# Performance work log

Hardware: AMD Instinct MI355X
Metric: run time of the kernel (lower is better)

## Reference

```python
import jax, jax.numpy as jnp
import numpy as np

HEADS = 8
DIM_HEAD = 64
SMOOTH = 1e-4
BN_EPS = 1e-5


def setup_inputs() -> dict:
    key = jax.random.key(0)
    k1, k2, k3 = jax.random.split(key, 3)
    B, C, H, W = 1, 256, 64, 64
    inner = HEADS * DIM_HEAD  # 512
    x = jax.random.normal(k1, (B, C, H, W), dtype=jnp.float32)
    # 1x1 conv weights stored as [out_ch, in_ch]
    w_qkv = jax.random.normal(k2, (3 * inner, C), dtype=jnp.float32) * (1.0 / np.sqrt(C))
    w_out = jax.random.normal(k3, (C, inner), dtype=jnp.float32) * (1.0 / np.sqrt(inner))
    gamma = jnp.ones((C,), dtype=jnp.float32)
    beta = jnp.zeros((C,), dtype=jnp.float32)
    return {"x": x, "w_qkv": w_qkv, "w_out": w_out, "gamma": gamma, "beta": beta}


def reference(x, w_qkv, w_out, gamma, beta):
    B, C, H, W = x.shape
    n = H * W
    # 1x1 conv == channel matmul: [B,3*inner,H,W]
    qkv = jnp.einsum('bchw,oc->bohw', x, w_qkv)
    q, k, v = jnp.split(qkv, 3, axis=1)

    def to_heads(t):
        # b (g d) h w -> b g (h w) d
        return t.reshape(B, HEADS, DIM_HEAD, n).transpose(0, 1, 3, 2)

    q, k, v = to_heads(q), to_heads(k), to_heads(v)
    # cosine-style normalized attention (no softmax)
    attn = jnp.einsum('bgnd,bgmd->bgnm', q, k)  # [B,g,n,n]
    qn = jnp.sqrt(jnp.sum(q * q, axis=-1) + SMOOTH)  # [B,g,n]
    kn = jnp.sqrt(jnp.sum(k * k, axis=-1) + SMOOTH)  # [B,g,n]
    attn = attn / (qn[:, :, :, None] * kn[:, :, None, :] + SMOOTH)
    out = jnp.einsum('bgnm,bgmd->bgnd', attn, v)  # [B,g,n,d]
    # b g (h w) d -> b (g d) h w
    out = out.transpose(0, 1, 3, 2).reshape(B, HEADS * DIM_HEAD, H, W)
    # projection conv 1x1 + BatchNorm2d (training stats) + ReLU
    out = jnp.einsum('bchw,oc->bohw', out, w_out)
    mean = jnp.mean(out, axis=(0, 2, 3), keepdims=True)
    var = jnp.var(out, axis=(0, 2, 3), keepdims=True)
    out = (out - mean) / jnp.sqrt(var + BN_EPS)
    out = out * gamma[None, :, None, None] + beta[None, :, None, None]
    return jax.nn.relu(out)
```

## Files before the change

### kernel.cpp

```cpp
#include <hip/hip_runtime.h>
#include <hip/hip_bf16.h>

#define NSP   4096
#define CIN   256
#define INNER 512
#define QKV_ROWS 1536

typedef __attribute__((ext_vector_type(8))) short bf16x8;
typedef __attribute__((ext_vector_type(4))) float f32x4;

__global__ __launch_bounds__(256) void conv_weights(
    const float* __restrict__ w_qkv, const float* __restrict__ w_out,
    __hip_bfloat16* __restrict__ dq, __hip_bfloat16* __restrict__ do_)
{
    const int gid = blockIdx.x * 256 + threadIdx.x;
    const int i = gid * 8;
    const float* src;
    __hip_bfloat16* dst;
    int off;
    if (i < QKV_ROWS * CIN) { src = w_qkv; dst = dq;  off = i; }
    else                    { src = w_out; dst = do_; off = i - QKV_ROWS * CIN; }
    const float4 a = *(const float4*)(src + off);
    const float4 b = *(const float4*)(src + off + 4);
    alignas(16) __hip_bfloat16 t[8];
    t[0] = __float2bfloat16(a.x); t[1] = __float2bfloat16(a.y);
    t[2] = __float2bfloat16(a.z); t[3] = __float2bfloat16(a.w);
    t[4] = __float2bfloat16(b.x); t[5] = __float2bfloat16(b.y);
    t[6] = __float2bfloat16(b.z); t[7] = __float2bfloat16(b.w);
    *(uint4*)(dst + off) = *(const uint4*)t;
}

__global__ __launch_bounds__(256) void transpose_convert(
    const float* __restrict__ x, __hip_bfloat16* __restrict__ xT)
{
    __shared__ float t[64][65];
    const int n0 = blockIdx.x * 64, c0 = blockIdx.y * 64;
    const int tid = threadIdx.x;
    const int cl = tid >> 2, nl0 = (tid & 3) * 16;
    #pragma unroll
    for (int j = 0; j < 4; ++j) {
        const float4 v = *(const float4*)(x + (size_t)(c0 + cl) * NSP + n0 + nl0 + j * 4);
        t[cl][nl0 + j*4 + 0] = v.x; t[cl][nl0 + j*4 + 1] = v.y;
        t[cl][nl0 + j*4 + 2] = v.z; t[cl][nl0 + j*4 + 3] = v.w;
    }
    __syncthreads();
    const int nr = tid >> 2, cc0 = (tid & 3) * 16;
    alignas(16) __hip_bfloat16 tmp[16];
    #pragma unroll
    for (int j = 0; j < 16; ++j) tmp[j] = __float2bfloat16(t[cc0 + j][nr]);
    __hip_bfloat16* d = xT + (size_t)(n0 + nr) * CIN + c0 + cc0;
    *(uint4*)(d)     = ((const uint4*)tmp)[0];
    *(uint4*)(d + 8) = ((const uint4*)tmp)[1];
}

template<int K, int BM, int FR, int DO_NORMS>
__global__ __launch_bounds__(256) void gemm_bf16(
    const __hip_bfloat16* __restrict__ A,
    const __hip_bfloat16* __restrict__ BT,
    __hip_bfloat16* __restrict__ C, int Nstride,
    float* __restrict__ inv_qn, float* __restrict__ inv_kn,
    __hip_bfloat16* __restrict__ qT)
{
    __shared__ __hip_bfloat16 smem[(BM + 128) * 64];
    __hip_bfloat16* As = smem;
    __hip_bfloat16* Bs = smem + BM * 64;
    const int tid = threadIdx.x;
    const int w = tid >> 6, l = tid & 63;
    const int wr = w >> 1, wc = w & 1;
    const int row0 = blockIdx.y * BM, col0 = blockIdx.x * 128;

    f32x4 acc[FR][4];
    #pragma unroll
    for (int i = 0; i < FR; ++i)
        #pragma unroll
        for (int j = 0; j < 4; ++j)
            acc[i][j] = (f32x4){0.f, 0.f, 0.f, 0.f};

    for (int kt = 0; kt < K; kt += 64) {
        #pragma unroll
        for (int i = 0; i < BM / 32; ++i) {
            const int o = i * 4096 + w * 1024 + l * 16;
            const int r_ = o >> 7;
            const int kel = ((o & 127) ^ ((r_ & 7) << 4)) >> 1;
            __builtin_amdgcn_global_load_lds(
                (const __attribute__((address_space(1))) void*)(A + (size_t)(row0 + r_) * K + kt + kel),
                (__attribute__((address_space(3))) void*)((char*)As + o),
                16, 0, 0);
        }
        #pragma unroll
        for (int i = 0; i < 4; ++i) {
            const int o = i * 4096 + w * 1024 + l * 16;
            const int r_ = o >> 7;
            const int kel = ((o & 127) ^ ((r_ & 7) << 4)) >> 1;
            __builtin_amdgcn_global_load_lds(
                (const __attribute__((address_space(1))) void*)(BT + (size_t)(col0 + r_) * K + kt + kel),
                (__attribute__((address_space(3))) void*)((char*)Bs + o),
                16, 0, 0);
        }
        __syncthreads();

        #pragma unroll
        for (int ks = 0; ks < 2; ++ks) {
            bf16x8 af[FR], bfr[4];
            #pragma unroll
            for (int fr = 0; fr < FR; ++fr) {
                const int row = wr * FR * 16 + fr * 16 + (l & 15);
                const int addr = row * 128 + ((ks * 64 + ((l >> 4) * 16)) ^ ((row & 7) << 4));
                af[fr] = *(const bf16x8*)((const char*)As + addr);
            }
            #pragma unroll
            for (int fc = 0; fc < 4; ++fc) {
                const int col = wc * 64 + fc * 16 + (l & 15);
                const int addr = col * 128 + ((ks * 64 + ((l >> 4) * 16)) ^ ((col & 7) << 4));
                bfr[fc] = *(const bf16x8*)((const char*)Bs + addr);
            }
            #pragma unroll
            for (int fr = 0; fr < FR; ++fr)
                #pragma unroll
                for (int fc = 0; fc < 4; ++fc)
                    acc[fr][fc] = __builtin_amdgcn_mfma_f32_16x16x32_bf16(
                        af[fr], bfr[fc], acc[fr][fc], 0, 0, 0);
        }
        __syncthreads();
    }

    #pragma unroll
    for (int fr = 0; fr < FR; ++fr)
        #pragma unroll
        for (int fc = 0; fc < 4; ++fc)
            #pragma unroll
            for (int r = 0; r < 4; ++r) {
                const int row = row0 + wr * FR * 16 + fr * 16 + (l >> 4) * 4 + r;
                const int col = col0 + wc * 64 + fc * 16 + (l & 15);
                C[(size_t)row * Nstride + col] = __float2bfloat16(acc[fr][fc][r]);
            }

    if constexpr (DO_NORMS) {
        const int chbase = row0 + wr * 64;
        if (chbase < 1024) {
            const int head = chbase >> 6;
            #pragma unroll
            for (int fc = 0; fc < 4; ++fc) {
                float s = 0.f;
                #pragma unroll
                for (int fr = 0; fr < FR; ++fr)
                    #pragma unroll
                    for (int r = 0; r < 4; ++r)
                        s += acc[fr][fc][r] * acc[fr][fc][r];
                s += __shfl_xor(s, 16, 64);
                s += __shfl_xor(s, 32, 64);
                if ((l >> 4) == 0) {
                    const int col = col0 + wc * 64 + fc * 16 + l;
                    const float inv = rsqrtf(s + 1e-4f);
                    if (head < 8) inv_qn[head * NSP + col] = inv;
                    else          inv_kn[(head - 8) * NSP + col] = inv;
                }
            }
        }
        if (chbase < 512) {
            #pragma unroll
            for (int fr = 0; fr < FR; ++fr)
                #pragma unroll
                for (int fc = 0; fc < 4; ++fc) {
                    const int rowb = chbase + fr * 16 + (l >> 4) * 4;
                    const int col  = col0 + wc * 64 + fc * 16 + (l & 15);
                    alignas(8) __hip_bfloat16 t4[4];
                    #pragma unroll
                    for (int r = 0; r < 4; ++r) t4[r] = __float2bfloat16(acc[fr][fc][r]);
                    *(unsigned long long*)(qT + (size_t)col * INNER + rowb) =
                        *(const unsigned long long*)t4;
                }
        }
    }
}

__device__ inline bf16x8 scale8(bf16x8 a, float4 s0, float4 s1) {
    union { bf16x8 v; unsigned short u[8]; } in, out;
    in.v = a;
    const float s[8] = {s0.x, s0.y, s0.z, s0.w, s1.x, s1.y, s1.z, s1.w};
    #pragma unroll
    for (int j = 0; j < 8; ++j) {
        const float f = __uint_as_float(((unsigned)(unsigned short)in.u[j]) << 16) * s[j];
        const __hip_bfloat16 h = __float2bfloat16(f);
        out.u[j] = *(const unsigned short*)&h;
    }
    return out.v;
}

__global__ __launch_bounds__(256) void s_mfma(
    const __hip_bfloat16* __restrict__ qkv, const float* __restrict__ inv_kn,
    float* __restrict__ S_part)
{
    const int c = blockIdx.x, g = blockIdx.y;
    const int tid = threadIdx.x;
    const int w = tid >> 6, l = tid & 63;
    const __hip_bfloat16* kb = qkv + (size_t)(512 + g * 64 + w * 16 + (l & 15)) * NSP;
    const float* ikn = inv_kn + g * NSP;

    f32x4 acc[4];
    #pragma unroll
    for (int j = 0; j < 4; ++j) acc[j] = (f32x4){0.f, 0.f, 0.f, 0.f};

    #pragma unroll
    for (int s8 = 0; s8 < 4; ++s8) {
        const int na = c * 128 + s8 * 32 + (l >> 4) * 8;
        bf16x8 a = *(const bf16x8*)(kb + na);
        const float4 i0 = *(const float4*)(ikn + na);
        const float4 i1 = *(const float4*)(ikn + na + 4);
        a = scale8(a, i0, i1);
        #pragma unroll
        for (int fc = 0; fc < 4; ++fc) {
            const bf16x8 b = *(const bf16x8*)(
                qkv + (size_t)(1024 + g * 64 + fc * 16 + (l & 15)) * NSP + na);
            acc[fc] = __builtin_amdgcn_mfma_f32_16x16x32_bf16(a, b, acc[fc], 0, 0, 0);
        }
    }
    float* out = S_part + (size_t)(c * 8 + g) * 4096;
    #pragma unroll
    for (int fc = 0; fc < 4; ++fc)
        #pragma unroll
        for (int r = 0; r < 4; ++r)
            out[(w * 16 + (l >> 4) * 4 + r) * 64 + fc * 16 + (l & 15)] = acc[fc][r];
}

__global__ __launch_bounds__(256) void s_reduce(
    const float* __restrict__ S_part, __hip_bfloat16* __restrict__ SbT)
{
    const int t = blockIdx.x * 256 + threadIdx.x;
    const int g = t >> 12, rem = t & 4095;
    const int d1 = rem >> 6, d2 = rem & 63;
    float s = 0.f;
    #pragma unroll
    for (int c = 0; c < 32; ++c)
        s += S_part[(size_t)(c * 8 + g) * 4096 + d1 * 64 + d2];
    SbT[g * 4096 + d2 * 64 + d1] = __float2bfloat16(s);
}

__global__ __launch_bounds__(256) void av_mfma(
    const __hip_bfloat16* __restrict__ qT, const float* __restrict__ inv_qn,
    const __hip_bfloat16* __restrict__ SbT, __hip_bfloat16* __restrict__ attnT)
{
    const int nb = blockIdx.x, g = blockIdx.y;
    const int tid = threadIdx.x;
    const int w = tid >> 6, l = tid & 63;
    const int nwave = nb * 256 + w * 64;

    bf16x8 bfr[2][4];
    #pragma unroll
    for (int ks = 0; ks < 2; ++ks)
        #pragma unroll
        for (int fc = 0; fc < 4; ++fc)
            bfr[ks][fc] = *(const bf16x8*)(
                SbT + g * 4096 + (fc * 16 + (l & 15)) * 64 + ks * 32 + (l >> 4) * 8);

    #pragma unroll
    for (int mr = 0; mr < 4; ++mr) {
        f32x4 acc[4];
        #pragma unroll
        for (int j = 0; j < 4; ++j) acc[j] = (f32x4){0.f, 0.f, 0.f, 0.f};
        #pragma unroll
        for (int ks = 0; ks < 2; ++ks) {
            const bf16x8 a = *(const bf16x8*)(
                qT + (size_t)(nwave + mr * 16 + (l & 15)) * INNER + g * 64 + ks * 32 + (l >> 4) * 8);
            #pragma unroll
            for (int fc = 0; fc < 4; ++fc)
                acc[fc] = __builtin_amdgcn_mfma_f32_16x16x32_bf16(a, bfr[ks][fc], acc[fc], 0, 0, 0);
        }
        const int nrow = nwave + mr * 16 + (l >> 4) * 4;
        const float4 iq = *(const float4*)(inv_qn + g * NSP + nrow);
        const float iqa[4] = {iq.x, iq.y, iq.z, iq.w};
        #pragma unroll
        for (int fc = 0; fc < 4; ++fc)
            #pragma unroll
            for (int r = 0; r < 4; ++r)
                attnT[(size_t)(nrow + r) * INNER + g * 64 + fc * 16 + (l & 15)] =
                    __float2bfloat16(acc[fc][r] * iqa[r]);
    }
}

__global__ __launch_bounds__(256) void bn_fused(
    const __hip_bfloat16* __restrict__ proj,
    const float* __restrict__ gamma, const float* __restrict__ beta,
    float* __restrict__ out)
{
    const int c = blockIdx.x;
    const int tid = threadIdx.x;
    const __hip_bfloat16* p = proj + (size_t)c * NSP + tid * 16;
    float v[16];
    {
        const uint4 u0 = *(const uint4*)(p);
        const uint4 u1 = *(const uint4*)(p + 8);
        const __hip_bfloat16* b0 = (const __hip_bfloat16*)&u0;
        const __hip_bfloat16* b1 = (const __hip_bfloat16*)&u1;
        #pragma unroll
        for (int j = 0; j < 8; ++j) { v[j] = __bfloat162float(b0[j]); v[8 + j] = __bfloat162float(b1[j]); }
    }
    float s = 0.f, q = 0.f;
    #pragma unroll
    for (int j = 0; j < 16; ++j) { s += v[j]; q += v[j] * v[j]; }
    #pragma unroll
    for (int m = 1; m < 64; m <<= 1) { s += __shfl_xor(s, m, 64); q += __shfl_xor(q, m, 64); }
    __shared__ float ss[4], qq[4];
    if ((tid & 63) == 0) { ss[tid >> 6] = s; qq[tid >> 6] = q; }
    __syncthreads();
    s = ss[0] + ss[1] + ss[2] + ss[3];
    q = qq[0] + qq[1] + qq[2] + qq[3];
    const float mean = s * (1.f / 4096.f);
    const float var  = q * (1.f / 4096.f) - mean * mean;
    const float scal = rsqrtf(var + 1e-5f) * gamma[c];
    const float bb   = beta[c];
    float* o = out + (size_t)c * NSP + tid * 16;
    #pragma unroll
    for (int j = 0; j < 16; j += 4) {
        float4 r;
        r.x = (v[j+0] - mean) * scal + bb; r.x = r.x > 0.f ? r.x : 0.f;
        r.y = (v[j+1] - mean) * scal + bb; r.y = r.y > 0.f ? r.y : 0.f;
        r.z = (v[j+2] - mean) * scal + bb; r.z = r.z > 0.f ? r.z : 0.f;
        r.w = (v[j+3] - mean) * scal + bb; r.w = r.w > 0.f ? r.w : 0.f;
        *(float4*)(o + j) = r;
    }
}

extern "C" void kernel_launch(void* const* d_in, const int* in_sizes, int n_in,
                              void* d_out, int out_size, void* d_ws, size_t ws_size,
                              hipStream_t stream)
{
    const float* x      = (const float*)d_in[0];
    const float* w_qkv  = (const float*)d_in[1];
    const float* w_out  = (const float*)d_in[2];
    const float* gamma  = (const float*)d_in[3];
    const float* beta   = (const float*)d_in[4];
    float* out = (float*)d_out;

    char* ws = (char*)d_ws;
    __hip_bfloat16* qkv_bf  = (__hip_bfloat16*)ws;
    __hip_bfloat16* xT_bf   = (__hip_bfloat16*)(ws + 12582912);
    __hip_bfloat16* wqkv_bf = (__hip_bfloat16*)(ws + 14680064);
    __hip_bfloat16* wout_bf = (__hip_bfloat16*)(ws + 15466496);
    __hip_bfloat16* attnT   = (__hip_bfloat16*)(ws + 15728640);
    __hip_bfloat16* proj_bf = (__hip_bfloat16*)(ws + 19922944);
    float* inv_qn           = (float*)(ws + 22020096);
    float* inv_kn           = (float*)(ws + 22151168);
    __hip_bfloat16* qT      = (__hip_bfloat16*)(ws + 22282240);
    float* S_part           = (float*)(ws + 26476544);
    __hip_bfloat16* SbT     = (__hip_bfloat16*)(ws + 30670848);

    conv_weights<<<(QKV_ROWS * CIN + CIN * INNER) / 2048, 256, 0, stream>>>(
        w_qkv, w_out, wqkv_bf, wout_bf);
    transpose_convert<<<dim3(NSP / 64, CIN / 64), 256, 0, stream>>>(x, xT_bf);

    gemm_bf16<CIN, 128, 4, 1><<<dim3(NSP / 128, QKV_ROWS / 128), 256, 0, stream>>>(
        wqkv_bf, xT_bf, qkv_bf, NSP, inv_qn, inv_kn, qT);

    s_mfma<<<dim3(32, 8), 256, 0, stream>>>(qkv_bf, inv_kn, S_part);

    s_reduce<<<128, 256, 0, stream>>>(S_part, SbT);

    av_mfma<<<dim3(16, 8), 256, 0, stream>>>(qT, inv_qn, SbT, attnT);

    gemm_bf16<INNER, 64, 2, 0><<<dim3(NSP / 128, CIN / 64), 256, 0, stream>>>(
        wout_bf, attnT, proj_bf, NSP, nullptr, nullptr, nullptr);

    bn_fused<<<CIN, 256, 0, stream>>>(proj_bf, gamma, beta, out);
}
```

Baseline: 105.5 us.

## Fold q/k norm scaling into QKV GEMM epilogue and merge prep kernels

Merges the weight-conversion and input-transpose kernels into a single prep launch. The q/k inverse norms are now applied directly in the QKV GEMM epilogue rather than written to separate buffers and reapplied in s_mfma and av_mfma. This removes the inv_qn/inv_kn buffers, their reads and the per-element rescale in s_mfma. s_mfma is also changed to use half as many blocks, each doing twice the work, so s_reduce sums 16 partials instead of 32. The trade-off is lower parallelism in s_mfma. Q/K are rounded to bf16 after scaling rather than before, and the dropped ‑1e-4 term in the denominator is ignored.

Result: no change. 104.3 us (-1.2%).

```diff
diff --git a/kernel.cpp b/kernel.cpp
--- a/kernel.cpp
+++ b/kernel.cpp
@@ -9,48 +9,48 @@
 typedef __attribute__((ext_vector_type(8))) short bf16x8;
 typedef __attribute__((ext_vector_type(4))) float f32x4;
 
-__global__ __launch_bounds__(256) void conv_weights(
-    const float* __restrict__ w_qkv, const float* __restrict__ w_out,
-    __hip_bfloat16* __restrict__ dq, __hip_bfloat16* __restrict__ do_)
-{
-    const int gid = blockIdx.x * 256 + threadIdx.x;
-    const int i = gid * 8;
-    const float* src;
-    __hip_bfloat16* dst;
-    int off;
-    if (i < QKV_ROWS * CIN) { src = w_qkv; dst = dq;  off = i; }
-    else                    { src = w_out; dst = do_; off = i - QKV_ROWS * CIN; }
-    const float4 a = *(const float4*)(src + off);
-    const float4 b = *(const float4*)(src + off + 4);
-    alignas(16) __hip_bfloat16 t[8];
-    t[0] = __float2bfloat16(a.x); t[1] = __float2bfloat16(a.y);
-    t[2] = __float2bfloat16(a.z); t[3] = __float2bfloat16(a.w);
-    t[4] = __float2bfloat16(b.x); t[5] = __float2bfloat16(b.y);
-    t[6] = __float2bfloat16(b.z); t[7] = __float2bfloat16(b.w);
-    *(uint4*)(dst + off) = *(const uint4*)t;
-}
-
-__global__ __launch_bounds__(256) void transpose_convert(
-    const float* __restrict__ x, __hip_bfloat16* __restrict__ xT)
+__global__ __launch_bounds__(256) void prep(
+    const float* __restrict__ x, const float* __restrict__ w_qkv,
+    const float* __restrict__ w_out,
+    __hip_bfloat16* __restrict__ xT, __hip_bfloat16* __restrict__ wq,
+    __hip_bfloat16* __restrict__ wo)
 {
     __shared__ float t[64][65];
-    const int n0 = blockIdx.x * 64, c0 = blockIdx.y * 64;
-    const int tid = threadIdx.x;
-    const int cl = tid >> 2, nl0 = (tid & 3) * 16;
-    #pragma unroll
-    for (int j = 0; j < 4; ++j) {
-        const float4 v = *(const float4*)(x + (size_t)(c0 + cl) * NSP + n0 + nl0 + j * 4);
-        t[cl][nl0 + j*4 + 0] = v.x; t[cl][nl0 + j*4 + 1] = v.y;
-        t[cl][nl0 + j*4 + 2] = v.z; t[cl][nl0 + j*4 + 3] = v.w;
-    }
-    __syncthreads();
-    const int nr = tid >> 2, cc0 = (tid & 3) * 16;
-    alignas(16) __hip_bfloat16 tmp[16];
-    #pragma unroll
-    for (int j = 0; j < 16; ++j) tmp[j] = __float2bfloat16(t[cc0 + j][nr]);
-    __hip_bfloat16* d = xT + (size_t)(n0 + nr) * CIN + c0 + cc0;
-    *(uint4*)(d)     = ((const uint4*)tmp)[0];
-    *(uint4*)(d + 8) = ((const uint4*)tmp)[1];
+    const int bx = blockIdx.x;
+    const int tid = threadIdx.x;
+    if (bx < 256) {
+        const int n0 = (bx & 63) * 64, c0 = (bx >> 6) * 64;
+        const int cl = tid >> 2, nl0 = (tid & 3) * 16;
+        #pragma unroll
+        for (int j = 0; j < 4; ++j) {
+            const float4 v = *(const float4*)(x + (size_t)(c0 + cl) * NSP + n0 + nl0 + j * 4);
+            t[cl][nl0 + j*4 + 0] = v.x; t[cl][nl0 + j*4 + 1] = v.y;
+            t[cl][nl0 + j*4 + 2] = v.z; t[cl][nl0 + j*4 + 3] = v.w;
+        }
+        __syncthreads();
+        const int nr = tid >> 2, cc0 = (tid & 3) * 16;
+        alignas(16) __hip_bfloat16 tmp[16];
+        #pragma unroll
+        for (int j = 0; j < 16; ++j) tmp[j] = __float2bfloat16(t[cc0 + j][nr]);
+        __hip_bfloat16* d = xT + (size_t)(n0 + nr) * CIN + c0 + cc0;
+        *(uint4*)(d)     = ((const uint4*)tmp)[0];
+        *(uint4*)(d + 8) = ((const uint4*)tmp)[1];
+    } else {
+        const int i = ((bx - 256) * 256 + tid) * 8;
+        const float* src;
+        __hip_bfloat16* dst;
+        int off;
+        if (i < QKV_ROWS * CIN) { src = w_qkv; dst = wq; off = i; }
+        else                    { src = w_out; dst = wo; off = i - QKV_ROWS * CIN; }
+        const float4 a = *(const float4*)(src + off);
+        const float4 b = *(const float4*)(src + off + 4);
+        alignas(16) __hip_bfloat16 tt[8];
+        tt[0] = __float2bfloat16(a.x); tt[1] = __float2bfloat16(a.y);
+        tt[2] = __float2bfloat16(a.z); tt[3] = __float2bfloat16(a.w);
+        tt[4] = __float2bfloat16(b.x); tt[5] = __float2bfloat16(b.y);
+        tt[6] = __float2bfloat16(b.z); tt[7] = __float2bfloat16(b.w);
+        *(uint4*)(dst + off) = *(const uint4*)tt;
+    }
 }
 
 template<int K, int BM, int FR, int DO_NORMS>
@@ -58,7 +58,6 @@
     const __hip_bfloat16* __restrict__ A,
     const __hip_bfloat16* __restrict__ BT,
     __hip_bfloat16* __restrict__ C, int Nstride,
-    float* __restrict__ inv_qn, float* __restrict__ inv_kn,
     __hip_bfloat16* __restrict__ qT)
 {
     __shared__ __hip_bfloat16 smem[(BM + 128) * 64];
@@ -124,21 +123,10 @@
         __syncthreads();
     }
 
-    #pragma unroll
-    for (int fr = 0; fr < FR; ++fr)
-        #pragma unroll
-        for (int fc = 0; fc < 4; ++fc)
-            #pragma unroll
-            for (int r = 0; r < 4; ++r) {
-                const int row = row0 + wr * FR * 16 + fr * 16 + (l >> 4) * 4 + r;
-                const int col = col0 + wc * 64 + fc * 16 + (l & 15);
-                C[(size_t)row * Nstride + col] = __float2bfloat16(acc[fr][fc][r]);
-            }
-
     if constexpr (DO_NORMS) {
         const int chbase = row0 + wr * 64;
+        float inv[4] = {1.f, 1.f, 1.f, 1.f};
         if (chbase < 1024) {
-            const int head = chbase >> 6;
             #pragma unroll
             for (int fc = 0; fc < 4; ++fc) {
                 float s = 0.f;
@@ -149,12 +137,7 @@
                         s += acc[fr][fc][r] * acc[fr][fc][r];
                 s += __shfl_xor(s, 16, 64);
                 s += __shfl_xor(s, 32, 64);
-                if ((l >> 4) == 0) {
-                    const int col = col0 + wc * 64 + fc * 16 + l;
-                    const float inv = rsqrtf(s + 1e-4f);
-                    if (head < 8) inv_qn[head * NSP + col] = inv;
-                    else          inv_kn[(head - 8) * NSP + col] = inv;
-                }
+                inv[fc] = rsqrtf(s + 1e-4f);
             }
         }
         if (chbase < 512) {
@@ -166,52 +149,58 @@
                     const int col  = col0 + wc * 64 + fc * 16 + (l & 15);
                     alignas(8) __hip_bfloat16 t4[4];
                     #pragma unroll
-                    for (int r = 0; r < 4; ++r) t4[r] = __float2bfloat16(acc[fr][fc][r]);
+                    for (int r = 0; r < 4; ++r)
+                        t4[r] = __float2bfloat16(acc[fr][fc][r] * inv[fc]);
                     *(unsigned long long*)(qT + (size_t)col * INNER + rowb) =
                         *(const unsigned long long*)t4;
                 }
-        }
-    }
-}
-
-__device__ inline bf16x8 scale8(bf16x8 a, float4 s0, float4 s1) {
-    union { bf16x8 v; unsigned short u[8]; } in, out;
-    in.v = a;
-    const float s[8] = {s0.x, s0.y, s0.z, s0.w, s1.x, s1.y, s1.z, s1.w};
-    #pragma unroll
-    for (int j = 0; j < 8; ++j) {
-        const float f = __uint_as_float(((unsigned)(unsigned short)in.u[j]) << 16) * s[j];
-        const __hip_bfloat16 h = __float2bfloat16(f);
-        out.u[j] = *(const unsigned short*)&h;
-    }
-    return out.v;
+        } else {
+            #pragma unroll
+            for (int fr = 0; fr < FR; ++fr)
+                #pragma unroll
+                for (int fc = 0; fc < 4; ++fc)
+                    #pragma unroll
+                    for (int r = 0; r < 4; ++r) {
+                        const int row = row0 + wr * FR * 16 + fr * 16 + (l >> 4) * 4 + r;
+                        const int col = col0 + wc * 64 + fc * 16 + (l & 15);
+                        C[(size_t)row * Nstride + col] =
+                            __float2bfloat16(acc[fr][fc][r] * inv[fc]);
+                    }
+        }
+    } else {
+        #pragma unroll
+        for (int fr = 0; fr < FR; ++fr)
+            #pragma unroll
+            for (int fc = 0; fc < 4; ++fc)
+                #pragma unroll
+                for (int r = 0; r < 4; ++r) {
+                    const int row = row0 + wr * FR * 16 + fr * 16 + (l >> 4) * 4 + r;
+                    const int col = col0 + wc * 64 + fc * 16 + (l & 15);
+                    C[(size_t)row * Nstride + col] = __float2bfloat16(acc[fr][fc][r]);
+                }
+    }
 }
 
 __global__ __launch_bounds__(256) void s_mfma(
-    const __hip_bfloat16* __restrict__ qkv, const float* __restrict__ inv_kn,
-    float* __restrict__ S_part)
+    const __hip_bfloat16* __restrict__ qkv, float* __restrict__ S_part)
 {
     const int c = blockIdx.x, g = blockIdx.y;
     const int tid = threadIdx.x;
     const int w = tid >> 6, l = tid & 63;
     const __hip_bfloat16* kb = qkv + (size_t)(512 + g * 64 + w * 16 + (l & 15)) * NSP;
-    const float* ikn = inv_kn + g * NSP;
+    const __hip_bfloat16* vb = qkv + (size_t)(1024 + g * 64 + (l & 15)) * NSP;
 
     f32x4 acc[4];
     #pragma unroll
     for (int j = 0; j < 4; ++j) acc[j] = (f32x4){0.f, 0.f, 0.f, 0.f};
 
     #pragma unroll
-    for (int s8 = 0; s8 < 4; ++s8) {
-        const int na = c * 128 + s8 * 32 + (l >> 4) * 8;
-        bf16x8 a = *(const bf16x8*)(kb + na);
-        const float4 i0 = *(const float4*)(ikn + na);
-        const float4 i1 = *(const float4*)(ikn + na + 4);
-        a = scale8(a, i0, i1);
+    for (int s8 = 0; s8 < 8; ++s8) {
+        const int na = c * 256 + s8 * 32 + (l >> 4) * 8;
+        const bf16x8 a = *(const bf16x8*)(kb + na);
         #pragma unroll
         for (int fc = 0; fc < 4; ++fc) {
-            const bf16x8 b = *(const bf16x8*)(
-                qkv + (size_t)(1024 + g * 64 + fc * 16 + (l & 15)) * NSP + na);
+            const bf16x8 b = *(const bf16x8*)(vb + (size_t)(fc * 16) * NSP + na);
             acc[fc] = __builtin_amdgcn_mfma_f32_16x16x32_bf16(a, b, acc[fc], 0, 0, 0);
         }
     }
@@ -231,13 +220,13 @@
     const int d1 = rem >> 6, d2 = rem & 63;
     float s = 0.f;
     #pragma unroll
-    for (int c = 0; c < 32; ++c)
+    for (int c = 0; c < 16; ++c)
         s += S_part[(size_t)(c * 8 + g) * 4096 + d1 * 64 + d2];
     SbT[g * 4096 + d2 * 64 + d1] = __float2bfloat16(s);
 }
 
 __global__ __launch_bounds__(256) void av_mfma(
-    const __hip_bfloat16* __restrict__ qT, const float* __restrict__ inv_qn,
+    const __hip_bfloat16* __restrict__ qT,
     const __hip_bfloat16* __restrict__ SbT, __hip_bfloat16* __restrict__ attnT)
 {
     const int nb = blockIdx.x, g = blockIdx.y;
@@ -267,14 +256,12 @@
                 acc[fc] = __builtin_amdgcn_mfma_f32_16x16x32_bf16(a, bfr[ks][fc], acc[fc], 0, 0, 0);
         }
         const int nrow = nwave + mr * 16 + (l >> 4) * 4;
-        const float4 iq = *(const float4*)(inv_qn + g * NSP + nrow);
-        const float iqa[4] = {iq.x, iq.y, iq.z, iq.w};
         #pragma unroll
         for (int fc = 0; fc < 4; ++fc)
             #pragma unroll
             for (int r = 0; r < 4; ++r)
                 attnT[(size_t)(nrow + r) * INNER + g * 64 + fc * 16 + (l & 15)] =
-                    __float2bfloat16(acc[fc][r] * iqa[r]);
+                    __float2bfloat16(acc[fc][r]);
     }
 }
 
@@ -339,27 +326,23 @@
     __hip_bfloat16* wout_bf = (__hip_bfloat16*)(ws + 15466496);
     __hip_bfloat16* attnT   = (__hip_bfloat16*)(ws + 15728640);
     __hip_bfloat16* proj_bf = (__hip_bfloat16*)(ws + 19922944);
-    float* inv_qn           = (float*)(ws + 22020096);
-    float* inv_kn           = (float*)(ws + 22151168);
     __hip_bfloat16* qT      = (__hip_bfloat16*)(ws + 22282240);
     float* S_part           = (float*)(ws + 26476544);
     __hip_bfloat16* SbT     = (__hip_bfloat16*)(ws + 30670848);
 
-    conv_weights<<<(QKV_ROWS * CIN + CIN * INNER) / 2048, 256, 0, stream>>>(
-        w_qkv, w_out, wqkv_bf, wout_bf);
-    transpose_convert<<<dim3(NSP / 64, CIN / 64), 256, 0, stream>>>(x, xT_bf);
+    prep<<<512, 256, 0, stream>>>(x, w_qkv, w_out, xT_bf, wqkv_bf, wout_bf);
 
     gemm_bf16<CIN, 128, 4, 1><<<dim3(NSP / 128, QKV_ROWS / 128), 256, 0, stream>>>(
-        wqkv_bf, xT_bf, qkv_bf, NSP, inv_qn, inv_kn, qT);
-
-    s_mfma<<<dim3(32, 8), 256, 0, stream>>>(qkv_bf, inv_kn, S_part);
+        wqkv_bf, xT_bf, qkv_bf, NSP, qT);
+
+    s_mfma<<<dim3(16, 8), 256, 0, stream>>>(qkv_bf, S_part);
 
     s_reduce<<<128, 256, 0, stream>>>(S_part, SbT);
 
-    av_mfma<<<dim3(16, 8), 256, 0, stream>>>(qT, inv_qn, SbT, attnT);
+    av_mfma<<<dim3(16, 8), 256, 0, stream>>>(qT, SbT, attnT);
 
     gemm_bf16<INNER, 64, 2, 0><<<dim3(NSP / 128, CIN / 64), 256, 0, stream>>>(
-        wout_bf, attnT, proj_bf, NSP, nullptr, nullptr, nullptr);
+        wout_bf, attnT, proj_bf, NSP, nullptr);
 
     bn_fused<<<CIN, 256, 0, stream>>>(proj_bf, gamma, beta, out);
 }
```
